# Optimization experiments

Hardware: AMD Instinct MI355X
Metric: run time of the kernel (lower is better)

Reference implementation:

```python
import jax, jax.numpy as jnp
import numpy as np

D_MODEL = 1024
NUM_HEADS = 16
MODULUS = 2147483647
B, S = 2, 2048


def setup_inputs() -> dict:
    key = jax.random.key(0)
    d = D_MODEL
    names_dims = [
        ('q_w', d, d), ('k_w', d, d), ('v_w', d, d), ('o_w', d, d),
        ('emb1_w', 1, d // 2), ('emb2_w', d // 2, d),
        ('log_w', 1, d // 4), ('prime_w', 10, d // 4),
        ('div_w', 20, d // 4), ('bit_w', 32, d // 4),
        ('fus_w', d, d),
    ]
    ks = jax.random.split(key, len(names_dims) + 3)
    inp = {}
    for (name, fin, fout), k in zip(names_dims, ks[:len(names_dims)]):
        inp[name] = jax.random.normal(k, (fin, fout), jnp.float32) * 0.02
        inp[name.replace('_w', '_b')] = jnp.zeros((fout,), jnp.float32)
    inp['arith_bias'] = jax.random.normal(ks[-3], (NUM_HEADS, 1, 1), jnp.float32)
    inp['gcd_weight'] = jnp.ones((1,), jnp.float32)
    inp['encodings'] = jax.random.randint(ks[-2], (B, S), 1, 1000000, dtype=jnp.int32)
    return inp


def reference(encodings, q_w, q_b, k_w, k_b, v_w, v_b, o_w, o_b,
              emb1_w, emb1_b, emb2_w, emb2_b, log_w, log_b,
              prime_w, prime_b, div_w, div_b, bit_w, bit_b,
              fus_w, fus_b, arith_bias, gcd_weight):
    Bz, Sz = encodings.shape
    d = q_w.shape[0]
    H = NUM_HEADS
    hd = d // H

    # --- ArithmeticEmbedding ---
    ef = encodings.astype(jnp.float32)
    norm = (ef / MODULUS)[..., None]                       # [B,S,1]
    base = jnp.maximum(norm @ emb1_w + emb1_b, 0.0) @ emb2_w + emb2_b
    logf = jnp.log(ef + 1.0)[..., None] @ log_w + log_b    # [B,S,d/4]
    primes = jnp.array([2, 3, 5, 7, 11, 13, 17, 19, 23, 29], dtype=jnp.int32)
    pf = (encodings[..., None] % primes == 0).astype(jnp.float32) @ prime_w + prime_b
    tv = jnp.arange(2, 22, dtype=jnp.int32)
    df = ((encodings[..., None] % tv).astype(jnp.float32) / tv.astype(jnp.float32)) @ div_w + div_b
    shifts = jnp.arange(32, dtype=jnp.int32)
    bf = (((encodings[..., None] >> shifts) & 1)).astype(jnp.float32) @ bit_w + bit_b
    feats = jnp.concatenate([logf, pf, df, bf], axis=-1)   # [B,S,d]
    hidden = base + feats @ fus_w + fus_b

    # --- ArithmeticAttention ---
    q = (hidden @ q_w + q_b).reshape(Bz, Sz, H, hd)
    k = (hidden @ k_w + k_b).reshape(Bz, Sz, H, hd)
    v = (hidden @ v_w + v_b).reshape(Bz, Sz, H, hd)
    scores = jnp.einsum('bihd,bjhd->bhij', q, k) / jnp.sqrt(jnp.float32(hd))
    # vectorized arithmetic bias (original is an O(S^2) python loop)
    ei = encodings[:, :, None]
    ej = encodings[:, None, :]
    gcd_approx = jnp.minimum(ei % (ej + 1), ej % (ei + 1)).astype(jnp.float32)
    bias = gcd_approx / (jnp.maximum(ei, ej) + 1).astype(jnp.float32)
    bias = jnp.where(jnp.eye(Sz, dtype=bool)[None], 0.0, bias)  # i==j -> 0
    scores = scores + bias[:, None] * gcd_weight + arith_bias
    attn = jax.nn.softmax(scores, axis=-1)
    out = jnp.einsum('bhij,bjhd->bihd', attn, v).reshape(Bz, Sz, d)
    return out @ o_w + o_b
```

## Files before the change

kernel.cpp:

```cpp
#include <hip/hip_runtime.h>
#include <hip/hip_bf16.h>

typedef unsigned short u16;
typedef __attribute__((ext_vector_type(8))) __bf16 bf16x8;
typedef __attribute__((ext_vector_type(4))) float f32x4;
typedef __attribute__((ext_vector_type(16))) float f32x16;

#define SEQ 2048
#define NB 2
#define NH 16
#define HD 64
#define DM 1024
#define LDQKV 3072
#define KF 576
#define LOG2E 1.4426950408889634f
#define NSPL 3

__device__ __forceinline__ u16 f2bf(float f) {
    unsigned u = __float_as_uint(f);
    unsigned r = u + 0x7FFFu + ((u >> 16) & 1u);
    return (u16)(r >> 16);
}
__device__ __forceinline__ float bf2f(u16 x) {
    return __uint_as_float(((unsigned)x) << 16);
}
__device__ __forceinline__ unsigned cvt_pk_bf16(float a, float b) {
    unsigned r;
    asm("v_cvt_pk_bf16_f32 %0, %1, %2" : "=v"(r) : "v"(a), "v"(b));
    return r;
}
__device__ __forceinline__ void gl_lds16(const u16* g, u16* l) {
    __builtin_amdgcn_global_load_lds((const __attribute__((address_space(1))) unsigned int*)g,
                                     (__attribute__((address_space(3))) unsigned int*)l, 16, 0, 0);
}
__device__ __forceinline__ unsigned fmod_u24(unsigned a, unsigned b) {
    float q = truncf(__fdividef((float)a, (float)b));
    int r = (int)a - (int)((unsigned)q * b);
    r += (r < 0) ? (int)b : 0;
    r -= (r >= (int)b) ? (int)b : 0;
    return (unsigned)r;
}

__global__ __launch_bounds__(256) void transw5_kernel(const float* __restrict__ q_w,
                                                      const float* __restrict__ k_w,
                                                      const float* __restrict__ v_w,
                                                      const float* __restrict__ o_w,
                                                      const float* __restrict__ emb2_w,
                                                      u16* __restrict__ WqkvT,
                                                      u16* __restrict__ WoT,
                                                      u16* __restrict__ Wc) {
    const int z = blockIdx.z;
    int tx = threadIdx.x, ty = threadIdx.y;
    if (z >= 4) {
        int blin = blockIdx.y * 32 + blockIdx.x;
        if (blin >= 512) return;
        int i = (blin * 256 + ty * 32 + tx) * 4;
        float4 v = *(const float4*)&emb2_w[i];
        uint2 o;
        o.x = cvt_pk_bf16(v.x, v.y);
        o.y = cvt_pk_bf16(v.z, v.w);
        *(uint2*)&Wc[i] = o;
        return;
    }
    __shared__ float tl[32][33];
    const float* src = (z == 0) ? q_w : (z == 1) ? k_w : (z == 2) ? v_w : o_w;
    u16* dst = (z < 3) ? WqkvT + (size_t)z * 1024 * DM : WoT;
    const float scale = (z == 0) ? 0.125f * LOG2E : 1.0f;
    int n = blockIdx.x * 32 + tx;
    int kbase = blockIdx.y * 32;
#pragma unroll
    for (int i = 0; i < 4; ++i)
        tl[ty + i * 8][tx] = src[(size_t)(kbase + ty + i * 8) * DM + n];
    __syncthreads();
    int k = kbase + tx;
#pragma unroll
    for (int i = 0; i < 4; ++i) {
        int n2 = blockIdx.x * 32 + ty + i * 8;
        dst[(size_t)n2 * DM + k] = f2bf(tl[tx][ty + i * 8] * scale);
    }
}

__global__ __launch_bounds__(256) void fold_kernel(const float* __restrict__ log_w,
                                                   const float* __restrict__ prime_w,
                                                   const float* __restrict__ div_w,
                                                   const float* __restrict__ bit_w,
                                                   const float* __restrict__ fus_w,
                                                   const float* __restrict__ emb2_b,
                                                   const float* __restrict__ fus_b,
                                                   const float* __restrict__ log_b,
                                                   const float* __restrict__ prime_b,
                                                   const float* __restrict__ div_b,
                                                   const float* __restrict__ bit_b,
                                                   u16* __restrict__ Wc) {
    const int r = blockIdx.y;
    const int n = blockIdx.x * 256 + threadIdx.x;
    if (r == 63) {
        float acc = emb2_b[n] + fus_b[n];
#pragma unroll 4
        for (int m = 0; m < 256; ++m) {
            acc += log_b[m]   * fus_w[(size_t)m * DM + n];
            acc += prime_b[m] * fus_w[(size_t)(256 + m) * DM + n];
            acc += div_b[m]   * fus_w[(size_t)(512 + m) * DM + n];
            acc += bit_b[m]   * fus_w[(size_t)(768 + m) * DM + n];
        }
        Wc[(size_t)575 * DM + n] = f2bf(acc);
        return;
    }
    const float* wrow; int chunk;
    if (r == 0)       { wrow = log_w;                 chunk = 0;   }
    else if (r < 11)  { wrow = prime_w + (r - 1) * 256; chunk = 256; }
    else if (r < 31)  { wrow = div_w + (r - 11) * 256;  chunk = 512; }
    else              { wrow = bit_w + (r - 31) * 256;  chunk = 768; }
    float acc = 0.f;
#pragma unroll 8
    for (int m = 0; m < 256; ++m)
        acc += wrow[m] * fus_w[(size_t)(chunk + m) * DM + n];
    Wc[(size_t)(512 + r) * DM + n] = f2bf(acc);
}

__global__ __launch_bounds__(256) void prep_kernel(const int* __restrict__ enc,
                                                   const float* __restrict__ gcd_w,
                                                   const float* __restrict__ emb1_w,
                                                   const float* __restrict__ emb1_b,
                                                   const float* __restrict__ q_b,
                                                   const float* __restrict__ k_b,
                                                   const float* __restrict__ v_b,
                                                   float* __restrict__ bias2,
                                                   u16* __restrict__ F,
                                                   float* __restrict__ qkvb) {
    const int bx = blockIdx.x, t = threadIdx.x;
    if (bx < 8192) {
        int vi = bx * 256 + t;
        int i  = vi & 2047;
        int rr = (vi >> 11) & 15;
        int jt = (vi >> 15) & 31;
        int b  = vi >> 20;
        int j0 = jt * 64 + rr * 4;
        unsigned ei = (unsigned)enc[b * SEQ + i];
        float scale = gcd_w[0] * LOG2E;
        int4 ej4 = *(const int4*)&enc[b * SEQ + j0];
        f32x4 o;
#pragma unroll
        for (int e = 0; e < 4; ++e) {
            unsigned ej = (unsigned)((e == 0) ? ej4.x : (e == 1) ? ej4.y : (e == 2) ? ej4.z : ej4.w);
            unsigned r1 = fmod_u24(ei, ej + 1u);
            unsigned r2 = fmod_u24(ej, ei + 1u);
            float gg = (float)min(r1, r2);
            float mx = (float)(max(ei, ej) + 1u);
            o[e] = (i == j0 + e) ? 0.f : __fdividef(gg, mx) * scale;
        }
        *(f32x4*)&bias2[(size_t)vi * 4] = o;
    } else if (bx < 12288) {
        const int tok = bx - 8192;
        int e = enc[tok];
        float ef = (float)e;
        float nrm = ef / 2147483647.0f;
        for (int k = t; k < 512; k += 256)
            F[(size_t)tok * KF + k] = f2bf(fmaxf(nrm * emb1_w[k] + emb1_b[k], 0.f));
        if (t < 64) {
            float v;
            if (t == 0) v = logf(ef + 1.f);
            else if (t < 11) {
                const int pr[10] = {2, 3, 5, 7, 11, 13, 17, 19, 23, 29};
                v = (e % pr[t - 1] == 0) ? 1.f : 0.f;
            } else if (t < 31) {
                int tv = t - 11 + 2;
                v = (float)(e % tv) / (float)tv;
            } else if (t < 63) {
                int sh = t - 31;
                v = (float)((e >> sh) & 1);
            } else v = 1.0f;
            F[(size_t)tok * KF + 512 + t] = f2bf(v);
        }
    } else {
        int i = (bx - 12288) * 256 + t;
        const float C1 = 0.125f * LOG2E;
        qkvb[i] = (i < 1024) ? q_b[i] * C1 : (i < 2048 ? k_b[i - 1024] : v_b[i - 2048]);
    }
}

template <int OUT_BF16, int TN, int HB>
__global__ __launch_bounds__(256) void gemm_kernel(const u16* __restrict__ A,
                                                   const u16* __restrict__ BT,
                                                   const float* __restrict__ bias,
                                                   void* __restrict__ Cv,
                                                   int M, int N, int K) {
    constexpr int FN = TN / 32;
    __shared__ u16 As[128 * 32];
    __shared__ u16 Bs[TN * 32];
    const int t = threadIdx.x;
    const int w = t >> 6, l = t & 63, lr = l & 15, lg = l >> 4;
    const int m0 = blockIdx.y * 128, n0 = blockIdx.x * TN;
    const int wm = (w >> 1) * 64, wn = (w & 1) * (TN / 2);
    const int srow = l >> 2, scol = (l & 3) * 8;

    const u16* gA = &A[(size_t)(m0 + w * 32 + srow) * K + scol];
    u16* lA = &As[w * 1024];
    const u16* gB;
    u16* lB;
    if (TN == 128) { gB = &BT[(size_t)(n0 + w * 32 + srow) * K + scol]; lB = &Bs[w * 1024]; }
    else           { gB = &BT[(size_t)(n0 + w * 16 + srow) * K + scol]; lB = &Bs[w * 512];  }

    f32x4 acc[4][FN] = {};
    for (int k0 = 0; k0 < K; k0 += 32) {
        __syncthreads();
        gl_lds16(gA + k0, lA);
        gl_lds16(gA + k0 + (size_t)16 * K, lA + 512);
        if (TN == 128) {
            gl_lds16(gB + k0, lB);
            gl_lds16(gB + k0 + (size_t)16 * K, lB + 512);
        } else {
            gl_lds16(gB + k0, lB);
        }
        __syncthreads();
        bf16x8 a[4], b[FN];
#pragma unroll
        for (int i = 0; i < 4; ++i) a[i] = *(const bf16x8*)&As[(wm + i * 16 + lr) * 32 + lg * 8];
#pragma unroll
        for (int j = 0; j < FN; ++j) b[j] = *(const bf16x8*)&Bs[(wn + j * 16 + lr) * 32 + lg * 8];
#pragma unroll
        for (int mi = 0; mi < 4; ++mi)
#pragma unroll
            for (int ni = 0; ni < FN; ++ni)
                acc[mi][ni] = __builtin_amdgcn_mfma_f32_16x16x32_bf16(a[mi], b[ni], acc[mi][ni], 0, 0, 0);
    }
#pragma unroll
    for (int mi = 0; mi < 4; ++mi)
#pragma unroll
        for (int ni = 0; ni < FN; ++ni)
#pragma unroll
            for (int r = 0; r < 4; ++r) {
                int row = m0 + wm + mi * 16 + lg * 4 + r;
                int col = n0 + wn + ni * 16 + lr;
                float v = acc[mi][ni][r] + (HB ? bias[col] : 0.f);
                if (OUT_BF16)
                    ((u16*)Cv)[(size_t)row * N + col] = f2bf(v);
                else
                    ((float*)Cv)[(size_t)row * N + col] = v;
            }
}

__global__ __launch_bounds__(256) void vtrans_kernel(const u16* __restrict__ qkv,
                                                     u16* __restrict__ vT) {
    __shared__ u16 tile[64][72];
    int t = threadIdx.x;
    int s0 = blockIdx.x * 64, h = blockIdx.y, b = blockIdx.z;
    int sr = t >> 2, sc = (t & 3) * 16;
    const int4* g = (const int4*)&qkv[(size_t)(b * SEQ + s0 + sr) * LDQKV + 2048 + h * HD + sc];
    int4 v0 = g[0], v1 = g[1];
    *(int4*)&tile[sr][sc] = v0;
    *(int4*)&tile[sr][sc + 8] = v1;
    __syncthreads();
    int dl = sr, j0 = sc;
    u16 tmp[16];
#pragma unroll
    for (int jj = 0; jj < 16; ++jj) tmp[jj] = tile[j0 + jj][dl];
    u16* out = &vT[(size_t)((b * NH + h) * HD + dl) * SEQ + s0 + j0];
    *(int4*)&out[0] = *(int4*)&tmp[0];
    *(int4*)&out[8] = *(int4*)&tmp[8];
}

#define KVB 64
#define SWZ(row, cb) ((((int)(row)) << 7) + (((int)(cb)) ^ ((((int)(row)) & 7) << 4)))

__global__ __launch_bounds__(256, 3) void attn_kernel(const u16* __restrict__ qkv,
                                                      const u16* __restrict__ vT,
                                                      const float* __restrict__ bias2,
                                                      u16* __restrict__ Opart,
                                                      float* __restrict__ Lp,
                                                      float* __restrict__ Mp) {
    __shared__ char smem[49152];
    const int t = threadIdx.x, w = t >> 6, l = t & 63;
    const int q5 = l & 31, hi = l >> 5;
    char* PlB = smem + 32768 + (w << 12);
    const int qt = blockIdx.x, h = blockIdx.y;
    const int b = blockIdx.z / NSPL, sp = blockIdx.z % NSPL;
    const int qrow = qt * 128 + w * 32 + q5;
    const int jt0 = sp * 11;
    const int NT  = (sp == 2) ? 10 : 11;
    const int j0s = jt0 * KVB;

    bf16x8 qf[4];
#pragma unroll
    for (int ks = 0; ks < 4; ++ks)
        qf[ks] = *(const bf16x8*)&qkv[(size_t)(b * SEQ + qrow) * LDQKV + h * HD + ks * 16 + hi * 8];

    const int sr = t >> 2, sc = (t & 3) * 16;
    const u16* gK = &qkv[(size_t)(b * SEQ + j0s + sr) * LDQKV + 1024 + h * HD + sc];
    const u16* gV = &vT[(size_t)((b * NH + h) * HD + sr) * SEQ + j0s + sc];
    const float* gBl = &bias2[((((size_t)b * 32 + jt0) * 16 + hi) * 2048 + qrow) * 4];

    int4 kr0 = *(const int4*)&gK[0], kr1 = *(const int4*)&gK[8];
    int4 vr0 = *(const int4*)&gV[0], vr1 = *(const int4*)&gV[8];
    f32x4 br[8];
#pragma unroll
    for (int c = 0; c < 2; ++c)
#pragma unroll
        for (int g = 0; g < 4; ++g)
            br[c * 4 + g] = *(const f32x4*)&gBl[(size_t)(8 * c + 2 * g) << 13];

    float m_s = -1e30f, l_s = 0.f;
    f32x16 acc2[2] = {};

    for (int lt = 0; lt < NT; ++lt) {
        char* KtB = smem + (lt & 1) * 16384;
        char* VtB = KtB + 8192;
        *(int4*)(KtB + SWZ(sr, (t & 3) * 32))      = kr0;
        *(int4*)(KtB + SWZ(sr, (t & 3) * 32 + 16)) = kr1;
        *(int4*)(VtB + SWZ(sr, (t & 3) * 32))      = vr0;
        *(int4*)(VtB + SWZ(sr, (t & 3) * 32 + 16)) = vr1;
        if (lt < NT - 1) {
            kr0 = *(const int4*)&gK[(size_t)(lt + 1) * KVB * LDQKV];
            kr1 = *(const int4*)&gK[(size_t)(lt + 1) * KVB * LDQKV + 8];
            vr0 = *(const int4*)&gV[(lt + 1) * KVB];
            vr1 = *(const int4*)&gV[(lt + 1) * KVB + 8];
        }
        __syncthreads();

        f32x16 s2[2];
#pragma unroll
        for (int c = 0; c < 2; ++c)
#pragma unroll
            for (int g = 0; g < 4; ++g)
#pragma unroll
                for (int e = 0; e < 4; ++e)
                    s2[c][g * 4 + e] = br[c * 4 + g][e];
        if (lt < NT - 1) {
            const float* nB = gBl + ((size_t)(lt + 1) << 17);
#pragma unroll
            for (int c = 0; c < 2; ++c)
#pragma unroll
                for (int g = 0; g < 4; ++g)
                    br[c * 4 + g] = *(const f32x4*)&nB[(size_t)(8 * c + 2 * g) << 13];
        }

        __builtin_amdgcn_s_setprio(1);
#pragma unroll
        for (int ks = 0; ks < 4; ++ks)
#pragma unroll
            for (int c = 0; c < 2; ++c) {
                bf16x8 kf = *(const bf16x8*)(KtB + SWZ(32 * c + q5, ks * 32 + hi * 16));
                s2[c] = __builtin_amdgcn_mfma_f32_32x32x16_bf16(kf, qf[ks], s2[c], 0, 0, 0);
            }
        __builtin_amdgcn_s_setprio(0);

        float tm = s2[0][0];
#pragma unroll
        for (int c = 0; c < 2; ++c)
#pragma unroll
            for (int r = 0; r < 16; ++r) tm = fmaxf(tm, s2[c][r]);
        tm = fmaxf(tm, __shfl_xor(tm, 32));

        if (__any(tm > m_s + 8.f)) {
            float mn = fmaxf(m_s, tm);
            float al = __builtin_exp2f(m_s - mn);
            l_s *= al;
            m_s = mn;
#pragma unroll
            for (int dc = 0; dc < 2; ++dc)
#pragma unroll
                for (int r = 0; r < 16; ++r) acc2[dc][r] *= al;
        }

        float ps = 0.f;
#pragma unroll
        for (int c = 0; c < 2; ++c)
#pragma unroll
            for (int r = 0; r < 16; ++r) {
                float p = __builtin_exp2f(s2[c][r] - m_s);
                s2[c][r] = p;
                ps += p;
            }
        ps += __shfl_xor(ps, 32);
        l_s += ps;

#pragma unroll
        for (int c = 0; c < 2; ++c)
#pragma unroll
            for (int g = 0; g < 4; ++g) {
                uint2 u;
                u.x = cvt_pk_bf16(s2[c][4 * g + 0], s2[c][4 * g + 1]);
                u.y = cvt_pk_bf16(s2[c][4 * g + 2], s2[c][4 * g + 3]);
                *(uint2*)(PlB + SWZ(q5, (32 * c + 8 * g + 4 * hi) * 2)) = u;
            }
        asm volatile("s_waitcnt lgkmcnt(0)" ::: "memory");
        __builtin_amdgcn_sched_barrier(0);

        __builtin_amdgcn_s_setprio(1);
#pragma unroll
        for (int ks = 0; ks < 4; ++ks) {
            bf16x8 pb = *(const bf16x8*)(PlB + SWZ(q5, ks * 32 + hi * 16));
#pragma unroll
            for (int dc = 0; dc < 2; ++dc) {
                bf16x8 vf = *(const bf16x8*)(VtB + SWZ(32 * dc + q5, ks * 32 + hi * 16));
                acc2[dc] = __builtin_amdgcn_mfma_f32_32x32x16_bf16(vf, pb, acc2[dc], 0, 0, 0);
            }
        }
        __builtin_amdgcn_s_setprio(0);
    }

    u16* orow = &Opart[(size_t)((sp * NB + b) * SEQ + qrow) * DM + h * HD];
#pragma unroll
    for (int dc = 0; dc < 2; ++dc)
#pragma unroll
        for (int g = 0; g < 4; ++g) {
            uint2 u;
            u.x = cvt_pk_bf16(acc2[dc][4 * g + 0], acc2[dc][4 * g + 1]);
            u.y = cvt_pk_bf16(acc2[dc][4 * g + 2], acc2[dc][4 * g + 3]);
            *(uint2*)&orow[32 * dc + 8 * g + 4 * hi] = u;
        }
    if (hi == 0) {
        size_t idx = ((size_t)(sp * NB + b) * SEQ + qrow) * NH + h;
        Lp[idx] = l_s;
        Mp[idx] = m_s;
    }
}

__global__ __launch_bounds__(256) void comb_kernel(const u16* __restrict__ Opart,
                                                   const float* __restrict__ Lp,
                                                   const float* __restrict__ Mp,
                                                   u16* __restrict__ attn_o) {
    int tid = blockIdx.x * 256 + threadIdx.x;
    int base = tid * 4;
    int b = base / (SEQ * DM);
    int rem = base - b * SEQ * DM;
    int i = rem / DM;
    int c = rem - i * DM;
    int h = c >> 6;
    size_t ix[3];
    float m[3], lv[3];
#pragma unroll
    for (int s = 0; s < 3; ++s) {
        ix[s] = ((size_t)(s * NB + b) * SEQ + i) * NH + h;
        m[s] = Mp[ix[s]];
        lv[s] = Lp[ix[s]];
    }
    float ms = fmaxf(fmaxf(m[0], m[1]), m[2]);
    float a0 = __builtin_exp2f(m[0] - ms);
    float a1 = __builtin_exp2f(m[1] - ms);
    float a2 = __builtin_exp2f(m[2] - ms);
    float inv = 1.f / (a0 * lv[0] + a1 * lv[1] + a2 * lv[2]);
    a0 *= inv; a1 *= inv; a2 *= inv;
    uint2 o0 = *(const uint2*)&Opart[((size_t)(0 * NB + b) * SEQ + i) * DM + c];
    uint2 o1 = *(const uint2*)&Opart[((size_t)(1 * NB + b) * SEQ + i) * DM + c];
    uint2 o2 = *(const uint2*)&Opart[((size_t)(2 * NB + b) * SEQ + i) * DM + c];
    float v0 = a0 * bf2f(o0.x & 0xFFFF) + a1 * bf2f(o1.x & 0xFFFF) + a2 * bf2f(o2.x & 0xFFFF);
    float v1 = a0 * bf2f(o0.x >> 16)    + a1 * bf2f(o1.x >> 16)    + a2 * bf2f(o2.x >> 16);
    float v2 = a0 * bf2f(o0.y & 0xFFFF) + a1 * bf2f(o1.y & 0xFFFF) + a2 * bf2f(o2.y & 0xFFFF);
    float v3 = a0 * bf2f(o0.y >> 16)    + a1 * bf2f(o1.y >> 16)    + a2 * bf2f(o2.y >> 16);
    uint2 u;
    u.x = cvt_pk_bf16(v0, v1);
    u.y = cvt_pk_bf16(v2, v3);
    *(uint2*)&attn_o[(size_t)(b * SEQ + i) * DM + c] = u;
}

extern "C" void kernel_launch(void* const* d_in, const int* in_sizes, int n_in,
                              void* d_out, int out_size, void* d_ws, size_t ws_size,
                              hipStream_t stream) {
    const float* q_w    = (const float*)d_in[0];
    const float* q_b    = (const float*)d_in[1];
    const float* k_w    = (const float*)d_in[2];
    const float* k_b    = (const float*)d_in[3];
    const float* v_w    = (const float*)d_in[4];
    const float* v_b    = (const float*)d_in[5];
    const float* o_w    = (const float*)d_in[6];
    const float* o_b    = (const float*)d_in[7];
    const float* emb1_w = (const float*)d_in[8];
    const float* emb1_b = (const float*)d_in[9];
    const float* emb2_w = (const float*)d_in[10];
    const float* emb2_b = (const float*)d_in[11];
    const float* log_w  = (const float*)d_in[12];
    const float* log_b  = (const float*)d_in[13];
    const float* prime_w= (const float*)d_in[14];
    const float* prime_b= (const float*)d_in[15];
    const float* div_w  = (const float*)d_in[16];
    const float* div_b  = (const float*)d_in[17];
    const float* bit_w  = (const float*)d_in[18];
    const float* bit_b  = (const float*)d_in[19];
    const float* fus_w  = (const float*)d_in[20];
    const float* fus_b  = (const float*)d_in[21];
    const float* gcd_weight = (const float*)d_in[23];
    const int*   enc    = (const int*)d_in[24];

    char* ws = (char*)d_ws;
    size_t off = 0;
    auto alloc = [&](size_t bytes) {
        char* p = ws + off;
        off += (bytes + 255) & ~size_t(255);
        return p;
    };
    u16*   WqkvT  = (u16*)alloc((size_t)3072 * DM * 2);
    u16*   WoT    = (u16*)alloc((size_t)DM * DM * 2);
    u16*   Wc     = (u16*)alloc((size_t)KF * DM * 2);
    u16*   W2T    = (u16*)alloc((size_t)3072 * KF * 2);
    float* qkvb   = (float*)alloc(3072 * 4);
    u16*   F      = (u16*)alloc((size_t)NB * SEQ * KF * 2);
    u16*   qkv    = (u16*)alloc((size_t)NB * SEQ * LDQKV * 2);
    u16*   vT     = (u16*)alloc((size_t)NB * NH * HD * SEQ * 2);
    float* bias2  = (float*)alloc((size_t)NB * SEQ * SEQ * 4);
    u16*   attn_o = (u16*)alloc((size_t)NB * SEQ * DM * 2);
    u16*   Opart  = (u16*)alloc((size_t)NSPL * NB * SEQ * DM * 2);
    float* Lp     = (float*)alloc((size_t)NSPL * NB * SEQ * NH * 4);
    float* Mp     = (float*)alloc((size_t)NSPL * NB * SEQ * NH * 4);
    (void)ws_size; (void)n_in; (void)in_sizes; (void)out_size;

    transw5_kernel<<<dim3(32, 32, 5), dim3(32, 8), 0, stream>>>(q_w, k_w, v_w, o_w, emb2_w,
                                                                WqkvT, WoT, Wc);
    fold_kernel<<<dim3(4, 64), 256, 0, stream>>>(log_w, prime_w, div_w, bit_w, fus_w,
                                                 emb2_b, fus_b, log_b, prime_b, div_b, bit_b, Wc);
    prep_kernel<<<12300, 256, 0, stream>>>(enc, gcd_weight, emb1_w, emb1_b, q_b, k_b, v_b,
                                           bias2, F, qkvb);
    gemm_kernel<1, 64, 0><<<dim3(KF / 64, 3072 / 128), 256, 0, stream>>>(WqkvT, Wc, nullptr, W2T,
                                                                         3072, KF, DM);
    gemm_kernel<1, 128, 1><<<dim3(3072 / 128, NB * SEQ / 128), 256, 0, stream>>>(F, W2T, qkvb, qkv,
                                                                                 NB * SEQ, 3072, KF);
    vtrans_kernel<<<dim3(SEQ / 64, NH, NB), 256, 0, stream>>>(qkv, vT);
    attn_kernel<<<dim3(SEQ / 128, NH, NB * NSPL), 256, 0, stream>>>(qkv, vT, bias2, Opart, Lp, Mp);
    comb_kernel<<<NB * SEQ * DM / 4 / 256, 256, 0, stream>>>(Opart, Lp, Mp, attn_o);
    gemm_kernel<0, 64, 1><<<dim3(DM / 64, NB * SEQ / 128), 256, 0, stream>>>(attn_o, WoT, o_b, d_out,
                                                                             NB * SEQ, DM, DM);
}
```

Before: 205.4 us.

## Split KV into two halves, alias P buffer into K/V LDS, raise occupancy

Reduces the split-KV factor from three to two, so each block walks 16 KV tiles and the combine kernel merges only two partials. The P staging buffer now reuses the idle half of the double-buffered K/V shared memory, which cuts LDS to 32KB. Bias register prefetching is removed in favour of direct loads each tile, so launch bounds can allow four blocks per CU. An extra barrier at the end of each iteration protects the aliased buffer, at the cost of more synchronisation and exposed bias-load latency.

```diff
diff --git a/kernel.cpp b/kernel.cpp
--- a/kernel.cpp
+++ b/kernel.cpp
@@ -14,7 +14,7 @@
 #define LDQKV 3072
 #define KF 576
 #define LOG2E 1.4426950408889634f
-#define NSPL 3
+#define NSPL 2
 
 __device__ __forceinline__ u16 f2bf(float f) {
     unsigned u = __float_as_uint(f);
@@ -263,21 +263,20 @@
 #define KVB 64
 #define SWZ(row, cb) ((((int)(row)) << 7) + (((int)(cb)) ^ ((((int)(row)) & 7) << 4)))
 
-__global__ __launch_bounds__(256, 3) void attn_kernel(const u16* __restrict__ qkv,
+__global__ __launch_bounds__(256, 4) void attn_kernel(const u16* __restrict__ qkv,
                                                       const u16* __restrict__ vT,
                                                       const float* __restrict__ bias2,
                                                       u16* __restrict__ Opart,
                                                       float* __restrict__ Lp,
                                                       float* __restrict__ Mp) {
-    __shared__ char smem[49152];
+    __shared__ char smem[32768];
     const int t = threadIdx.x, w = t >> 6, l = t & 63;
     const int q5 = l & 31, hi = l >> 5;
-    char* PlB = smem + 32768 + (w << 12);
     const int qt = blockIdx.x, h = blockIdx.y;
-    const int b = blockIdx.z / NSPL, sp = blockIdx.z % NSPL;
+    const int b = blockIdx.z >> 1, sp = blockIdx.z & 1;
     const int qrow = qt * 128 + w * 32 + q5;
-    const int jt0 = sp * 11;
-    const int NT  = (sp == 2) ? 10 : 11;
+    const int jt0 = sp * 16;
+    const int NT  = 16;
     const int j0s = jt0 * KVB;
 
     bf16x8 qf[4];
@@ -292,12 +291,6 @@
 
     int4 kr0 = *(const int4*)&gK[0], kr1 = *(const int4*)&gK[8];
     int4 vr0 = *(const int4*)&gV[0], vr1 = *(const int4*)&gV[8];
-    f32x4 br[8];
-#pragma unroll
-    for (int c = 0; c < 2; ++c)
-#pragma unroll
-        for (int g = 0; g < 4; ++g)
-            br[c * 4 + g] = *(const f32x4*)&gBl[(size_t)(8 * c + 2 * g) << 13];
 
     float m_s = -1e30f, l_s = 0.f;
     f32x16 acc2[2] = {};
@@ -305,6 +298,7 @@
     for (int lt = 0; lt < NT; ++lt) {
         char* KtB = smem + (lt & 1) * 16384;
         char* VtB = KtB + 8192;
+        char* PlB = smem + (((lt + 1) & 1) << 14) + (w << 12);
         *(int4*)(KtB + SWZ(sr, (t & 3) * 32))      = kr0;
         *(int4*)(KtB + SWZ(sr, (t & 3) * 32 + 16)) = kr1;
         *(int4*)(VtB + SWZ(sr, (t & 3) * 32))      = vr0;
@@ -318,21 +312,13 @@
         __syncthreads();
 
         f32x16 s2[2];
+        const float* tB = gBl + ((size_t)lt << 17);
 #pragma unroll
         for (int c = 0; c < 2; ++c)
 #pragma unroll
             for (int g = 0; g < 4; ++g)
-#pragma unroll
-                for (int e = 0; e < 4; ++e)
-                    s2[c][g * 4 + e] = br[c * 4 + g][e];
-        if (lt < NT - 1) {
-            const float* nB = gBl + ((size_t)(lt + 1) << 17);
-#pragma unroll
-            for (int c = 0; c < 2; ++c)
-#pragma unroll
-                for (int g = 0; g < 4; ++g)
-                    br[c * 4 + g] = *(const f32x4*)&nB[(size_t)(8 * c + 2 * g) << 13];
-        }
+                *(f32x4*)((float*)&s2[c] + 4 * g) =
+                    *(const f32x4*)&tB[(size_t)(8 * c + 2 * g) << 13];
 
         __builtin_amdgcn_s_setprio(1);
 #pragma unroll
@@ -397,6 +383,7 @@
             }
         }
         __builtin_amdgcn_s_setprio(0);
+        __syncthreads();
     }
 
     u16* orow = &Opart[(size_t)((sp * NB + b) * SEQ + qrow) * DM + h * HD];
@@ -427,27 +414,20 @@
     int i = rem / DM;
     int c = rem - i * DM;
     int h = c >> 6;
-    size_t ix[3];
-    float m[3], lv[3];
-#pragma unroll
-    for (int s = 0; s < 3; ++s) {
-        ix[s] = ((size_t)(s * NB + b) * SEQ + i) * NH + h;
-        m[s] = Mp[ix[s]];
-        lv[s] = Lp[ix[s]];
-    }
-    float ms = fmaxf(fmaxf(m[0], m[1]), m[2]);
-    float a0 = __builtin_exp2f(m[0] - ms);
-    float a1 = __builtin_exp2f(m[1] - ms);
-    float a2 = __builtin_exp2f(m[2] - ms);
-    float inv = 1.f / (a0 * lv[0] + a1 * lv[1] + a2 * lv[2]);
-    a0 *= inv; a1 *= inv; a2 *= inv;
-    uint2 o0 = *(const uint2*)&Opart[((size_t)(0 * NB + b) * SEQ + i) * DM + c];
-    uint2 o1 = *(const uint2*)&Opart[((size_t)(1 * NB + b) * SEQ + i) * DM + c];
-    uint2 o2 = *(const uint2*)&Opart[((size_t)(2 * NB + b) * SEQ + i) * DM + c];
-    float v0 = a0 * bf2f(o0.x & 0xFFFF) + a1 * bf2f(o1.x & 0xFFFF) + a2 * bf2f(o2.x & 0xFFFF);
-    float v1 = a0 * bf2f(o0.x >> 16)    + a1 * bf2f(o1.x >> 16)    + a2 * bf2f(o2.x >> 16);
-    float v2 = a0 * bf2f(o0.y & 0xFFFF) + a1 * bf2f(o1.y & 0xFFFF) + a2 * bf2f(o2.y & 0xFFFF);
-    float v3 = a0 * bf2f(o0.y >> 16)    + a1 * bf2f(o1.y >> 16)    + a2 * bf2f(o2.y >> 16);
+    size_t ix1 = ((size_t)b * SEQ + i) * NH + h;
+    size_t ix2 = ((size_t)(NB + b) * SEQ + i) * NH + h;
+    float m1 = Mp[ix1], m2 = Mp[ix2];
+    float l1 = Lp[ix1], l2 = Lp[ix2];
+    float ms = fmaxf(m1, m2);
+    float a1 = __builtin_exp2f(m1 - ms), a2 = __builtin_exp2f(m2 - ms);
+    float inv = 1.f / (a1 * l1 + a2 * l2);
+    a1 *= inv; a2 *= inv;
+    uint2 o1 = *(const uint2*)&Opart[((size_t)b * SEQ + i) * DM + c];
+    uint2 o2 = *(const uint2*)&Opart[((size_t)(NB + b) * SEQ + i) * DM + c];
+    float v0 = a1 * bf2f(o1.x & 0xFFFF) + a2 * bf2f(o2.x & 0xFFFF);
+    float v1 = a1 * bf2f(o1.x >> 16)    + a2 * bf2f(o2.x >> 16);
+    float v2 = a1 * bf2f(o1.y & 0xFFFF) + a2 * bf2f(o2.y & 0xFFFF);
+    float v3 = a1 * bf2f(o1.y >> 16)    + a2 * bf2f(o2.y >> 16);
     uint2 u;
     u.x = cvt_pk_bf16(v0, v1);
     u.y = cvt_pk_bf16(v2, v3);
```

Measured after the change: 214.9 us. 4.6% more time.
